# Kernel tuning notes

Measured on AMD Instinct MI355X. Metric: run time of the kernel, lower is better.

Reference implementation:

```python
import jax, jax.numpy as jnp
import numpy as np


def setup_inputs() -> dict:
    key = jax.random.key(0)
    ks = jax.random.split(key, 6)
    B, N, d = 4096, 32768, 512
    return {
        "X_src": jax.random.normal(ks[0], (B, d), dtype=jnp.float32),
        "X_trans": jax.random.normal(ks[1], (B, d), dtype=jnp.float32),
        "Y_tgt": jax.random.normal(ks[2], (B, d), dtype=jnp.float32),
        "Z_src": jax.random.normal(ks[3], (N, d), dtype=jnp.float32),
        "Z_trans": jax.random.normal(ks[4], (N, d), dtype=jnp.float32),
        "Z_tgt": jax.random.normal(ks[5], (N, d), dtype=jnp.float32),
        "knn": 10,
    }


def _getknn(sc, k):
    # torch: topk(10) indices[:, :k], gather, sum  ==  sum of top-k values per row
    vals, _ = jax.lax.top_k(sc, k)  # [rows, k]
    return vals.sum() / k


def reference(X_src, X_trans, Y_tgt, Z_src, Z_trans, Z_tgt, knn):
    B = X_src.shape[0]
    f = 2.0 * (X_trans * Y_tgt).sum()
    # sc0: [B, N] similarity of translated src words vs target vocab
    fk0 = _getknn(X_trans @ Z_tgt.T, knn)
    # Z_trans.mm(Y_tgt.t()).t() == Y_tgt @ Z_trans.T : [B, N]
    fk1 = _getknn(Y_tgt @ Z_trans.T, knn)
    f = f - fk0 - fk1
    return -f / B
```

## Files before the change

kernel.cpp:

```cpp
#include <hip/hip_runtime.h>
#include <hip/hip_bf16.h>
#include <float.h>
#include <cstdint>


#define B_ROWS 4096
#define N_COLS 32768
#define D_K    512
#define NCHUNK (N_COLS / 128)

typedef __bf16 bf16x8 __attribute__((ext_vector_type(8)));
typedef float  f32x4  __attribute__((ext_vector_type(4)));
typedef unsigned short u16x2 __attribute__((ext_vector_type(2)));

__device__ __forceinline__ unsigned short f2bf(float f) {
    unsigned int u = __float_as_uint(f);
    u += 0x7FFFu + ((u >> 16) & 1u);
    return (unsigned short)(u >> 16);
}
__device__ __forceinline__ unsigned f2sort32(float f) {
    unsigned u = __float_as_uint(f);
    u += 0x7FFFu + ((u >> 16) & 1u);
    return u ^ (0x80000000u | (unsigned)((int)u >> 31));
}
__device__ __forceinline__ float sort2f(unsigned int y) {
    unsigned int x = (y & 0x8000u) ? (y ^ 0x8000u) : (~y & 0xFFFFu);
    return __uint_as_float(x << 16);
}
__device__ __forceinline__ unsigned umax(unsigned a, unsigned b) { return a > b ? a : b; }
__device__ __forceinline__ unsigned umin(unsigned a, unsigned b) { return a < b ? a : b; }

__device__ __forceinline__ void gload_lds16(const void* g, void* l) {
    __builtin_amdgcn_global_load_lds(
        (const __attribute__((address_space(1))) unsigned int*)(uintptr_t)g,
        (__attribute__((address_space(3))) unsigned int*)(uintptr_t)l,
        16, 0, 0);
}

__global__ void zero_scalars(float* sc) {
    if (threadIdx.x < 3) sc[threadIdx.x] = 0.0f;
}

__global__ void prep_kernel(const float4* __restrict__ X,
                            const float4* __restrict__ Y,
                            const float4* __restrict__ Zt,
                            const float4* __restrict__ Ztr,
                            ushort4* __restrict__ A0, ushort4* __restrict__ A1,
                            ushort4* __restrict__ B0, ushort4* __restrict__ B1,
                            float* __restrict__ dotacc) {
    const int z = blockIdx.y;
    int i = blockIdx.x * 256 + threadIdx.x;
    const int stride = gridDim.x * 256;
    if (z == 0) {
        float s = 0.0f;
        for (; i < B_ROWS * D_K / 4; i += stride) {
            float4 x = X[i], y = Y[i];
            ushort4 u; u.x = f2bf(x.x); u.y = f2bf(x.y);
            u.z = f2bf(x.z); u.w = f2bf(x.w);
            A0[i] = u;
            s += x.x * y.x + x.y * y.y + x.z * y.z + x.w * y.w;
        }
        for (int o = 32; o > 0; o >>= 1) s += __shfl_down(s, o);
        __shared__ float wsum[4];
        int lane = threadIdx.x & 63, w = threadIdx.x >> 6;
        if (lane == 0) wsum[w] = s;
        __syncthreads();
        if (threadIdx.x == 0)
            atomicAdd(dotacc, wsum[0] + wsum[1] + wsum[2] + wsum[3]);
    } else {
        const float4* src = (z == 1) ? Y : (z == 2) ? Zt : Ztr;
        ushort4* dst = (z == 1) ? A1 : (z == 2) ? B0 : B1;
        int n4 = (z == 1) ? (B_ROWS * D_K / 4) : (N_COLS * D_K / 4);
        for (; i < n4; i += stride) {
            float4 f = src[i];
            ushort4 u; u.x = f2bf(f.x); u.y = f2bf(f.y);
            u.z = f2bf(f.z); u.w = f2bf(f.w);
            dst[i] = u;
        }
    }
}

#define BARRIER()  asm volatile("s_barrier" ::: "memory")
#define VMCNT(N)   asm volatile("s_waitcnt vmcnt(" #N ")" ::: "memory")
#define LGKM(N)    asm volatile("s_waitcnt lgkmcnt(" #N ")" ::: "memory")
#define MEMFENCE() asm volatile("" ::: "memory")

#define STAGE(T) do { \
    gload_lds16(gA0 + (T) * 32, smem + ((T) & 3) * 16384 + w * 512); \
    gload_lds16(gA1 + (T) * 32, smem + ((T) & 3) * 16384 + (8 + w) * 512); \
    gload_lds16(gB0 + (T) * 32, smem + ((T) & 3) * 16384 + 8192 + w * 512); \
    gload_lds16(gB1 + (T) * 32, smem + ((T) & 3) * 16384 + 8192 + (8 + w) * 512); \
} while (0)

#define LOAD_AF(ARR, SLOT) { _Pragma("unroll") for (int mi = 0; mi < 8; ++mi) \
    ARR[mi] = *(const bf16x8*)(smem + (SLOT) * 16384 + abase + mi * 512 + lane8); }

#define MFMA32(ARR) { __builtin_amdgcn_s_setprio(1); \
    _Pragma("unroll") for (int mi = 0; mi < 8; ++mi) { \
    _Pragma("unroll") for (int ni = 0; ni < 4; ++ni) { \
        acc[mi][ni] = __builtin_amdgcn_mfma_f32_16x16x32_bf16( \
            bfr[ni], ARR[mi], acc[mi][ni], 0, 0, 0); } } \
    __builtin_amdgcn_s_setprio(0); }

#define KSTEP(J) do { \
    bf16x8 bfr[4]; \
    _Pragma("unroll") for (int ni = 0; ni < 4; ++ni) \
        bfr[ni] = *(const bf16x8*)(smem + ((J) & 3) * 16384 + bbase + ni * 512 + lane8); \
    MEMFENCE(); \
    if ((J) & 1) { \
        if ((J) < 15) LOAD_AF(af0, ((J) + 1) & 3) \
        MFMA32(af1) \
    } else { \
        if ((J) < 15) LOAD_AF(af1, ((J) + 1) & 3) \
        MFMA32(af0) \
    } \
    if ((J) < 12)       { LGKM(8); BARRIER(); STAGE((J) + 4); VMCNT(8); BARRIER(); } \
    else if ((J) == 12) { VMCNT(4); BARRIER(); } \
    else if ((J) == 13) { VMCNT(0); BARRIER(); } \
} while (0)

#define CSWAP(a, b) { unsigned _hi = umax(a, b), _lo = umin(a, b); a = _hi; b = _lo; }
#define SORT4() { CSWAP(m0, m1); CSWAP(m2, m3); CSWAP(m0, m2); CSWAP(m1, m3); CSWAP(m1, m2); }
#define INS(V) { u16x2 _hi; \
    _hi = __builtin_elementwise_max(t0, V); V = __builtin_elementwise_min(t0, V); t0 = _hi; \
    _hi = __builtin_elementwise_max(t1, V); V = __builtin_elementwise_min(t1, V); t1 = _hi; \
    _hi = __builtin_elementwise_max(t2, V); V = __builtin_elementwise_min(t2, V); t2 = _hi; \
    _hi = __builtin_elementwise_max(t3, V); V = __builtin_elementwise_min(t3, V); t3 = _hi; }

__global__ __launch_bounds__(512, 2)
void gemm_topk_kernel(const unsigned short* __restrict__ A0g,
                      const unsigned short* __restrict__ A1g,
                      const unsigned short* __restrict__ B0g,
                      const unsigned short* __restrict__ B1g,
                      uint2* __restrict__ P0, uint2* __restrict__ P1) {
    const unsigned short* A  = blockIdx.y ? A1g : A0g;
    const unsigned short* Bm = blockIdx.y ? B1g : B0g;
    uint2* P2 = blockIdx.y ? P1 : P0;

    __shared__ __align__(128) unsigned short smem[4 * 16384];

    const int tid   = threadIdx.x;
    const int lane  = tid & 63;
    const int w     = tid >> 6;
    const int wm    = w >> 2;
    const int wn    = w & 3;
    const int quad  = lane >> 4;
    const int mrow  = lane & 15;
    const int lane8 = lane * 8;

    const int b      = blockIdx.x;
    const int xcd    = b & 7;
    const int ii     = b >> 3;
    const int cw     = ii & 7;
    const int rowblk = (ii >> 3) & 15;
    const int cg     = ii >> 7;
    const int bn     = xcd * 16 + cg * 8 + cw;
    const int row0   = rowblk * 256;
    const int col0   = bn * 256;

    const unsigned short* gA0 = A  + (size_t)(row0 + w * 16 + mrow) * D_K + quad * 8;
    const unsigned short* gA1 = gA0 + 128 * D_K;
    const unsigned short* gB0 = Bm + (size_t)(col0 + w * 16 + mrow) * D_K + quad * 8;
    const unsigned short* gB1 = gB0 + 128 * D_K;

    const int abase = wm * 4096;
    const int bbase = 8192 + wn * 2048;

    f32x4 acc[8][4];
    #pragma unroll
    for (int mi = 0; mi < 8; ++mi)
        #pragma unroll
        for (int ni = 0; ni < 4; ++ni)
            acc[mi][ni] = (f32x4){0.f, 0.f, 0.f, 0.f};

    bf16x8 af0[8], af1[8];

    STAGE(0); MEMFENCE();
    STAGE(1); MEMFENCE();
    STAGE(2); MEMFENCE();
    STAGE(3);
    VMCNT(8);
    BARRIER();
    LOAD_AF(af0, 0)

    KSTEP(0);  KSTEP(1);  KSTEP(2);  KSTEP(3);
    KSTEP(4);  KSTEP(5);  KSTEP(6);  KSTEP(7);
    KSTEP(8);  KSTEP(9);  KSTEP(10); KSTEP(11);
    KSTEP(12); KSTEP(13); KSTEP(14); KSTEP(15);

    const int chunk = bn * 2 + (wn >> 1);
    const int half  = wn & 1;
    #pragma unroll
    for (int mi = 0; mi < 8; ++mi) {
        u16x2 t0 = {0, 0}, t1 = {0, 0}, t2 = {0, 0}, t3 = {0, 0};
        #pragma unroll
        for (int ni = 0; ni < 4; ++ni) {
            unsigned s0 = f2sort32(acc[mi][ni][0]);
            unsigned s1 = f2sort32(acc[mi][ni][1]);
            unsigned s2 = f2sort32(acc[mi][ni][2]);
            unsigned s3 = f2sort32(acc[mi][ni][3]);
            unsigned pa = (s0 >> 16) | (s1 & 0xFFFF0000u);
            unsigned pb = (s2 >> 16) | (s3 & 0xFFFF0000u);
            u16x2 v0 = *(u16x2*)&pa;
            u16x2 v1 = *(u16x2*)&pb;
            INS(v0); INS(v1);
        }
        unsigned m0 = umax((unsigned)t0.x, (unsigned)t3.y);
        unsigned m1 = umax((unsigned)t1.x, (unsigned)t2.y);
        unsigned m2 = umax((unsigned)t2.x, (unsigned)t1.y);
        unsigned m3 = umax((unsigned)t3.x, (unsigned)t0.y);
        SORT4();
        #pragma unroll
        for (int st = 0; st < 2; ++st) {
            unsigned pa = m0 | (m1 << 16);
            unsigned pb = m2 | (m3 << 16);
            unsigned qa = (unsigned)__shfl_xor((int)pa, st ? 32 : 16);
            unsigned qb = (unsigned)__shfl_xor((int)pb, st ? 32 : 16);
            unsigned ra = (qa >> 16) | (qa << 16);
            unsigned rb = (qb >> 16) | (qb << 16);
            u16x2 n0 = __builtin_elementwise_max(*(u16x2*)&pa, *(u16x2*)&rb);
            u16x2 n1 = __builtin_elementwise_max(*(u16x2*)&pb, *(u16x2*)&ra);
            m0 = n0.x; m1 = n0.y; m2 = n1.x; m3 = n1.y;
            SORT4();
        }
        if (quad == 0) {
            int row_g = row0 + wm * 128 + mi * 16 + mrow;
            P2[((size_t)row_g * NCHUNK + chunk) * 2 + half] =
                make_uint2(m0 | (m1 << 16), m2 | (m3 << 16));
        }
    }
}

__global__ __launch_bounds__(256, 4)
void merge_topk_kernel(const unsigned int* __restrict__ P0,
                       const unsigned int* __restrict__ P1,
                       float* __restrict__ sc) {
    const int g    = blockIdx.y;
    const int lane = threadIdx.x & 63;
    const int w    = threadIdx.x >> 6;
    const int row  = blockIdx.x * 4 + w;
    const unsigned int* Rp = (g ? P1 : P0) + (size_t)row * (NCHUNK * 4);

    u16x2 t[10];
    #pragma unroll
    for (int i = 0; i < 10; ++i) t[i] = (u16x2){0, 0};
    #pragma unroll 4
    for (int it = 0; it < 16; ++it) {
        unsigned int raw = Rp[lane + 64 * it];
        u16x2 v = *(u16x2*)&raw;
        #pragma unroll
        for (int i = 0; i < 10; ++i) {
            u16x2 hi = __builtin_elementwise_max(t[i], v);
            v = __builtin_elementwise_min(t[i], v);
            t[i] = hi;
        }
    }
    unsigned int wreg[10];
    #pragma unroll
    for (int i = 0; i < 10; ++i) {
        unsigned int mv = umax((unsigned int)t[i].x,
                               (unsigned int)t[9 - i].y);
        wreg[i] = (mv << 16) | ((unsigned int)lane << 4) | (unsigned int)i;
    }
    float sum10 = 0.0f;
    #pragma unroll
    for (int iter = 0; iter < 10; ++iter) {
        unsigned int mx = wreg[0];
        #pragma unroll
        for (int s = 1; s < 10; ++s) mx = umax(mx, wreg[s]);
        #pragma unroll
        for (int o = 32; o > 0; o >>= 1)
            mx = umax(mx, (unsigned int)__shfl_xor((int)mx, o));
        sum10 += sort2f(mx >> 16);
        #pragma unroll
        for (int s = 0; s < 10; ++s)
            if (wreg[s] == mx) wreg[s] = 0u;
    }
    if (lane == 0) atomicAdd(sc + 1 + g, sum10);
}

__global__ void finalize_kernel(const float* __restrict__ sc,
                                float* __restrict__ out) {
    if (threadIdx.x == 0) {
        float f = (sc[1] * 0.1f + sc[2] * 0.1f - 2.0f * sc[0]) * (1.0f / 4096.0f);
        out[0] = f;
    }
}

extern "C" void kernel_launch(void* const* d_in, const int* in_sizes, int n_in,
                              void* d_out, int out_size, void* d_ws, size_t ws_size,
                              hipStream_t stream) {
    const float* X_trans = (const float*)d_in[1];
    const float* Y_tgt   = (const float*)d_in[2];
    const float* Z_trans = (const float*)d_in[4];
    const float* Z_tgt   = (const float*)d_in[5];

    char* ws = (char*)d_ws;
    float* sc = (float*)ws;
    unsigned short* A0 = (unsigned short*)(ws + 256);
    unsigned short* A1 = A0 + (size_t)B_ROWS * D_K;
    unsigned short* B0 = A1 + (size_t)B_ROWS * D_K;
    unsigned short* B1 = B0 + (size_t)N_COLS * D_K;
    uint2* P0 = (uint2*)(B1 + (size_t)N_COLS * D_K);
    uint2* P1 = P0 + (size_t)B_ROWS * NCHUNK * 2;

    zero_scalars<<<1, 64, 0, stream>>>(sc);

    dim3 pgrid(2048, 4);
    prep_kernel<<<pgrid, 256, 0, stream>>>(
        (const float4*)X_trans, (const float4*)Y_tgt,
        (const float4*)Z_tgt, (const float4*)Z_trans,
        (ushort4*)A0, (ushort4*)A1, (ushort4*)B0, (ushort4*)B1, sc + 0);

    dim3 ggrid(2048, 2);
    gemm_topk_kernel<<<ggrid, 512, 0, stream>>>(A0, A1, B0, B1, P0, P1);

    dim3 mgrid(B_ROWS / 4, 2);
    merge_topk_kernel<<<mgrid, 256, 0, stream>>>(
        (const unsigned int*)P0, (const unsigned int*)P1, sc);

    finalize_kernel<<<1, 64, 0, stream>>>(sc, (float*)d_out);
}
```

Measured before the change: 683.5 us.

## Switch GEMM-topk to 32x32x16 MFMA with half-step double buffering

Replaces the 16x16x32 bf16 MFMA tiling with 32x32x16 MFMA tiles, changing the LDS staging layout, the fragment loads and the accumulator shape to 4x2 f32x16. The K loop now splits each stage into two half-steps with ping-pong A/B fragment registers and compiler sched barriers in place of explicit lgkm waits. The top-k epilogue is adapted to the new accumulator layout and needs one fewer cross-lane shuffle stage. The aim is fewer MFMA instructions and LDS reads per FLOP, at the risk of a changed register footprint and different LDS bank conflicts.

New measurement: 695.3 us. No clear change (+1.7%).

```diff
diff --git a/kernel.cpp b/kernel.cpp
--- a/kernel.cpp
+++ b/kernel.cpp
@@ -10,7 +10,7 @@
 #define NCHUNK (N_COLS / 128)
 
 typedef __bf16 bf16x8 __attribute__((ext_vector_type(8)));
-typedef float  f32x4  __attribute__((ext_vector_type(4)));
+typedef float  f32x16 __attribute__((ext_vector_type(16)));
 typedef unsigned short u16x2 __attribute__((ext_vector_type(2)));
 
 __device__ __forceinline__ unsigned short f2bf(float f) {
@@ -82,39 +82,38 @@
 
 #define BARRIER()  asm volatile("s_barrier" ::: "memory")
 #define VMCNT(N)   asm volatile("s_waitcnt vmcnt(" #N ")" ::: "memory")
-#define LGKM(N)    asm volatile("s_waitcnt lgkmcnt(" #N ")" ::: "memory")
-#define MEMFENCE() asm volatile("" ::: "memory")
+#define SCHEDB()   __builtin_amdgcn_sched_barrier(0)
 
 #define STAGE(T) do { \
-    gload_lds16(gA0 + (T) * 32, smem + ((T) & 3) * 16384 + w * 512); \
-    gload_lds16(gA1 + (T) * 32, smem + ((T) & 3) * 16384 + (8 + w) * 512); \
-    gload_lds16(gB0 + (T) * 32, smem + ((T) & 3) * 16384 + 8192 + w * 512); \
-    gload_lds16(gB1 + (T) * 32, smem + ((T) & 3) * 16384 + 8192 + (8 + w) * 512); \
+    gload_lds16(gA + (T) * 32,      smem + ((T) & 3) * 16384 + (w * 2 + 0) * 512); \
+    gload_lds16(gA + (T) * 32 + 16, smem + ((T) & 3) * 16384 + (w * 2 + 1) * 512); \
+    gload_lds16(gB + (T) * 32,      smem + ((T) & 3) * 16384 + 8192 + (w * 2 + 0) * 512); \
+    gload_lds16(gB + (T) * 32 + 16, smem + ((T) & 3) * 16384 + 8192 + (w * 2 + 1) * 512); \
 } while (0)
 
-#define LOAD_AF(ARR, SLOT) { _Pragma("unroll") for (int mi = 0; mi < 8; ++mi) \
-    ARR[mi] = *(const bf16x8*)(smem + (SLOT) * 16384 + abase + mi * 512 + lane8); }
-
-#define MFMA32(ARR) { __builtin_amdgcn_s_setprio(1); \
-    _Pragma("unroll") for (int mi = 0; mi < 8; ++mi) { \
-    _Pragma("unroll") for (int ni = 0; ni < 4; ++ni) { \
-        acc[mi][ni] = __builtin_amdgcn_mfma_f32_16x16x32_bf16( \
-            bfr[ni], ARR[mi], acc[mi][ni], 0, 0, 0); } } \
+#define LOADH(AF, BF, SLOT, KK) { \
+    _Pragma("unroll") for (int rb = 0; rb < 4; ++rb) \
+        AF[rb] = *(const bf16x8*)(smem + (SLOT) * 16384 + ((wm * 4 + rb) * 2 + (KK)) * 512 + lane8); \
+    _Pragma("unroll") for (int cb = 0; cb < 2; ++cb) \
+        BF[cb] = *(const bf16x8*)(smem + (SLOT) * 16384 + 8192 + ((wn * 2 + cb) * 2 + (KK)) * 512 + lane8); \
+}
+
+#define MFMAH(AF, BF) { __builtin_amdgcn_s_setprio(1); \
+    _Pragma("unroll") for (int rb = 0; rb < 4; ++rb) { \
+    _Pragma("unroll") for (int cb = 0; cb < 2; ++cb) { \
+        acc[rb][cb] = __builtin_amdgcn_mfma_f32_32x32x16_bf16( \
+            BF[cb], AF[rb], acc[rb][cb], 0, 0, 0); } } \
     __builtin_amdgcn_s_setprio(0); }
 
 #define KSTEP(J) do { \
-    bf16x8 bfr[4]; \
-    _Pragma("unroll") for (int ni = 0; ni < 4; ++ni) \
-        bfr[ni] = *(const bf16x8*)(smem + ((J) & 3) * 16384 + bbase + ni * 512 + lane8); \
-    MEMFENCE(); \
-    if ((J) & 1) { \
-        if ((J) < 15) LOAD_AF(af0, ((J) + 1) & 3) \
-        MFMA32(af1) \
-    } else { \
-        if ((J) < 15) LOAD_AF(af1, ((J) + 1) & 3) \
-        MFMA32(af0) \
-    } \
-    if ((J) < 12)       { LGKM(8); BARRIER(); STAGE((J) + 4); VMCNT(8); BARRIER(); } \
+    LOADH(afn, bfn, (J) & 3, 1); \
+    SCHEDB(); \
+    MFMAH(afc, bfc); \
+    if ((J) < 15) LOADH(afc, bfc, ((J) + 1) & 3, 0); \
+    SCHEDB(); \
+    MFMAH(afn, bfn); \
+    SCHEDB(); \
+    if ((J) < 12)       { VMCNT(4); BARRIER(); STAGE((J) + 4); } \
     else if ((J) == 12) { VMCNT(4); BARRIER(); } \
     else if ((J) == 13) { VMCNT(0); BARRIER(); } \
 } while (0)
@@ -144,8 +143,8 @@
     const int w     = tid >> 6;
     const int wm    = w >> 2;
     const int wn    = w & 3;
-    const int quad  = lane >> 4;
-    const int mrow  = lane & 15;
+    const int rlane = lane & 31;
+    const int hi    = lane >> 5;
     const int lane8 = lane * 8;
 
     const int b      = blockIdx.x;
@@ -158,30 +157,27 @@
     const int row0   = rowblk * 256;
     const int col0   = bn * 256;
 
-    const unsigned short* gA0 = A  + (size_t)(row0 + w * 16 + mrow) * D_K + quad * 8;
-    const unsigned short* gA1 = gA0 + 128 * D_K;
-    const unsigned short* gB0 = Bm + (size_t)(col0 + w * 16 + mrow) * D_K + quad * 8;
-    const unsigned short* gB1 = gB0 + 128 * D_K;
-
-    const int abase = wm * 4096;
-    const int bbase = 8192 + wn * 2048;
-
-    f32x4 acc[8][4];
-    #pragma unroll
-    for (int mi = 0; mi < 8; ++mi)
-        #pragma unroll
-        for (int ni = 0; ni < 4; ++ni)
-            acc[mi][ni] = (f32x4){0.f, 0.f, 0.f, 0.f};
-
-    bf16x8 af0[8], af1[8];
-
-    STAGE(0); MEMFENCE();
-    STAGE(1); MEMFENCE();
-    STAGE(2); MEMFENCE();
+    const unsigned short* gA = A  + (size_t)(row0 + w * 32 + rlane) * D_K + hi * 8;
+    const unsigned short* gB = Bm + (size_t)(col0 + w * 32 + rlane) * D_K + hi * 8;
+
+    f32x16 acc[4][2];
+    #pragma unroll
+    for (int rb = 0; rb < 4; ++rb)
+        #pragma unroll
+        for (int cb = 0; cb < 2; ++cb)
+            #pragma unroll
+            for (int e = 0; e < 16; ++e)
+                acc[rb][cb][e] = 0.0f;
+
+    bf16x8 afc[4], afn[4], bfc[2], bfn[2];
+
+    STAGE(0);
+    STAGE(1);
+    STAGE(2);
     STAGE(3);
     VMCNT(8);
     BARRIER();
-    LOAD_AF(af0, 0)
+    LOADH(afc, bfc, 0, 0)
 
     KSTEP(0);  KSTEP(1);  KSTEP(2);  KSTEP(3);
     KSTEP(4);  KSTEP(5);  KSTEP(6);  KSTEP(7);
@@ -191,40 +187,38 @@
     const int chunk = bn * 2 + (wn >> 1);
     const int half  = wn & 1;
     #pragma unroll
-    for (int mi = 0; mi < 8; ++mi) {
+    for (int rb = 0; rb < 4; ++rb) {
         u16x2 t0 = {0, 0}, t1 = {0, 0}, t2 = {0, 0}, t3 = {0, 0};
         #pragma unroll
-        for (int ni = 0; ni < 4; ++ni) {
-            unsigned s0 = f2sort32(acc[mi][ni][0]);
-            unsigned s1 = f2sort32(acc[mi][ni][1]);
-            unsigned s2 = f2sort32(acc[mi][ni][2]);
-            unsigned s3 = f2sort32(acc[mi][ni][3]);
-            unsigned pa = (s0 >> 16) | (s1 & 0xFFFF0000u);
-            unsigned pb = (s2 >> 16) | (s3 & 0xFFFF0000u);
-            u16x2 v0 = *(u16x2*)&pa;
-            u16x2 v1 = *(u16x2*)&pb;
-            INS(v0); INS(v1);
+        for (int cb = 0; cb < 2; ++cb) {
+            #pragma unroll
+            for (int p = 0; p < 8; ++p) {
+                unsigned sa = f2sort32(acc[rb][cb][2 * p]);
+                unsigned sb = f2sort32(acc[rb][cb][2 * p + 1]);
+                unsigned pk = (sa >> 16) | (sb & 0xFFFF0000u);
+                u16x2 v = *(u16x2*)&pk;
+                INS(v);
+            }
         }
         unsigned m0 = umax((unsigned)t0.x, (unsigned)t3.y);
         unsigned m1 = umax((unsigned)t1.x, (unsigned)t2.y);
         unsigned m2 = umax((unsigned)t2.x, (unsigned)t1.y);
         unsigned m3 = umax((unsigned)t3.x, (unsigned)t0.y);
         SORT4();
-        #pragma unroll
-        for (int st = 0; st < 2; ++st) {
+        {
             unsigned pa = m0 | (m1 << 16);
             unsigned pb = m2 | (m3 << 16);
-            unsigned qa = (unsigned)__shfl_xor((int)pa, st ? 32 : 16);
-            unsigned qb = (unsigned)__shfl_xor((int)pb, st ? 32 : 16);
+            unsigned qa = (unsigned)__shfl_xor((int)pa, 32);
+            unsigned qb = (unsigned)__shfl_xor((int)pb, 32);
             unsigned ra = (qa >> 16) | (qa << 16);
-            unsigned rb = (qb >> 16) | (qb << 16);
-            u16x2 n0 = __builtin_elementwise_max(*(u16x2*)&pa, *(u16x2*)&rb);
+            unsigned rb2 = (qb >> 16) | (qb << 16);
+            u16x2 n0 = __builtin_elementwise_max(*(u16x2*)&pa, *(u16x2*)&rb2);
             u16x2 n1 = __builtin_elementwise_max(*(u16x2*)&pb, *(u16x2*)&ra);
             m0 = n0.x; m1 = n0.y; m2 = n1.x; m3 = n1.y;
             SORT4();
         }
-        if (quad == 0) {
-            int row_g = row0 + wm * 128 + mi * 16 + mrow;
+        if (hi == 0) {
+            int row_g = row0 + wm * 128 + rb * 32 + rlane;
             P2[((size_t)row_g * NCHUNK + chunk) * 2 + half] =
                 make_uint2(m0 | (m1 << 16), m2 | (m3 << 16));
         }
```
